# Performance work log

Hardware: AMD Instinct MI355X
Metric: run time of the kernel (lower is better)

The kernel has to match this reference:

```python
import jax, jax.numpy as jnp
import numpy as np


def setup_inputs() -> dict:
    key = jax.random.key(0)
    k1, k2, k3 = jax.random.split(key, 3)
    B, C, H, W = 16, 64, 256, 256
    x = jax.random.normal(k1, (B, C, H, W), dtype=jnp.float32)
    g = jax.random.normal(k2, (B, C, H, W), dtype=jnp.float32)
    gamma = jax.random.normal(k3, (1,), dtype=jnp.float32)
    return {"x": x, "g": g, "gamma": gamma}


def reference(x, g, gamma):
    # x, g: (B, C, H, W); gamma: (1,)
    B, C, H, W = x.shape
    N = H * W
    xq = x.reshape(B, C, N)   # proj_query / proj_value
    gq = g.reshape(B, C, N)

    # channel-channel energy from x: (B, C, C)
    energy = jnp.einsum('bcn,bdn->bcd', xq, xq)
    attention = jax.nn.softmax(energy, axis=-1)

    # channel-channel energy from guide g: (B, C, C)
    energy_guide = jnp.einsum('bcn,bdn->bcd', gq, gq)
    attention_guide = jax.nn.softmax(energy_guide, axis=-1)

    # chained attention: (B, C, C)
    guide_energy = jnp.einsum('bcd,bde->bce', attention, attention_guide)
    guide_energy_new = jnp.max(guide_energy, axis=-1, keepdims=True) - guide_energy
    guide_attention = jax.nn.softmax(guide_energy_new, axis=-1)

    # apply to values and residual
    out = jnp.einsum('bcd,bdn->bcn', guide_attention, xq).reshape(B, C, H, W)
    return gamma[0] * out + x
```

## Files before the change

### kernel.cpp

```cpp
#include <hip/hip_runtime.h>


typedef _Float16 h8 __attribute__((ext_vector_type(8)));
typedef float    f4 __attribute__((ext_vector_type(4)));
typedef __fp16   p2 __attribute__((ext_vector_type(2)));
typedef unsigned long long ull;

#define NB 16
#define NC 64
#define NPIX 65536
#define GRAM_CHUNK 1024
#define PASS_PX 128
#define NPASS (GRAM_CHUNK / PASS_PX)
#define NCHUNK (NPIX / GRAM_CHUNK)
#define ROW_H 136
#define LDS_H (64 * ROW_H + 64)

#define AP_NPX 256
#define XT_ROW 72

__device__ __forceinline__ int rowbase_h(int c) {
    return c * ROW_H + (c >> 3) * 8;
}

__device__ __forceinline__ unsigned int pk(float a, float b) {
    p2 v = __builtin_amdgcn_cvt_pkrtz(a, b);
    return __builtin_bit_cast(unsigned int, v);
}

__global__ __launch_bounds__(256, 6) void gram_kernel(
    const float* __restrict__ x, const float* __restrict__ g,
    float* __restrict__ part)
{
    __shared__ __align__(16) _Float16 buf[LDS_H];

    const int tid = threadIdx.x;
    const int mtx = blockIdx.z;
    const float* src = (mtx ? g : x)
        + (size_t)blockIdx.y * NC * NPIX + (size_t)blockIdx.x * GRAM_CHUNK;

    const int w     = tid >> 6;
    const int lane  = tid & 63;
    const int l15   = lane & 15;
    const int khalf = lane >> 4;
    const int abase_h = rowbase_h(w * 16 + l15);

    const int sq = tid & 31;
    const int sr = tid >> 5;

    f4 acc[4];
    #pragma unroll
    for (int cb = 0; cb < 4; ++cb) acc[cb] = (f4){0.f, 0.f, 0.f, 0.f};

    for (int pass = 0; pass < NPASS; ++pass) {
        const float* ps = src + pass * PASS_PX;
        #pragma unroll
        for (int it = 0; it < 8; ++it) {
            int r = it * 8 + sr;
            f4 v = *(const f4*)(ps + (size_t)r * NPIX + sq * 4);
            ull h = (ull)pk(v.x, v.y) | ((ull)pk(v.z, v.w) << 32);
            *reinterpret_cast<ull*>(&buf[rowbase_h(r) + 4 * sq]) = h;
        }
        __syncthreads();

        #pragma unroll
        for (int ks = 0; ks < 4; ++ks) {
            int koff = ks * 32 + khalf * 8;
            h8 a = *reinterpret_cast<const h8*>(&buf[abase_h + koff]);
            #pragma unroll
            for (int cb = 0; cb < 4; ++cb) {
                h8 bf = *reinterpret_cast<const h8*>(&buf[rowbase_h(cb * 16 + l15) + koff]);
                acc[cb] = __builtin_amdgcn_mfma_f32_16x16x32_f16(a, bf, acc[cb], 0, 0, 0);
            }
        }
        __syncthreads();
    }

    float* po = part + (((size_t)blockIdx.x * NB + blockIdx.y) * 2 + mtx) * 4096;
    #pragma unroll
    for (int cb = 0; cb < 4; ++cb)
        #pragma unroll
        for (int r = 0; r < 4; ++r)
            po[(w * 16 + khalf * 4 + r) * 64 + cb * 16 + l15] = acc[cb][r];
}

__global__ __launch_bounds__(256) void reduce_kernel(
    const float* __restrict__ part, float* __restrict__ ex, float* __restrict__ eg)
{
    const int idx = blockIdx.x * 256 + threadIdx.x;
    const int bm = idx >> 12;
    const int cd = idx & 4095;
    float s = 0.f;
    #pragma unroll 8
    for (int ch = 0; ch < NCHUNK; ++ch)
        s += part[(size_t)ch * (NB * 2 * 4096) + (size_t)bm * 4096 + cd];
    float* dst = (bm & 1) ? eg : ex;
    dst[(bm >> 1) * 4096 + cd] = s;
}

__global__ __launch_bounds__(256) void chain_kernel(
    const float* __restrict__ ex, const float* __restrict__ eg,
    const float* __restrict__ gammap, float* __restrict__ M)
{
    __shared__ float A1[64][68];
    __shared__ float A2[64][68];
    __shared__ float red[64][4];

    const int b = blockIdx.x;
    const int tid = threadIdx.x;

    if (tid < 64) {
        const int c = tid;
        float r[64];
        #pragma unroll
        for (int d = 0; d < 64; ++d) r[d] = ex[b * 4096 + c * 64 + d];
        float mx = r[0];
        #pragma unroll
        for (int d = 1; d < 64; ++d) mx = fmaxf(mx, r[d]);
        float s = 0.f;
        #pragma unroll
        for (int d = 0; d < 64; ++d) { r[d] = expf(r[d] - mx); s += r[d]; }
        float inv = 1.f / s;
        #pragma unroll
        for (int d = 0; d < 64; ++d) A1[c][d] = r[d] * inv;

        #pragma unroll
        for (int d = 0; d < 64; ++d) r[d] = eg[b * 4096 + c * 64 + d];
        mx = r[0];
        #pragma unroll
        for (int d = 1; d < 64; ++d) mx = fmaxf(mx, r[d]);
        s = 0.f;
        #pragma unroll
        for (int d = 0; d < 64; ++d) { r[d] = expf(r[d] - mx); s += r[d]; }
        inv = 1.f / s;
        #pragma unroll
        for (int d = 0; d < 64; ++d) A2[c][d] = r[d] * inv;
    }
    __syncthreads();

    const int c = tid >> 2, sq = tid & 3;
    float ge[16];
    #pragma unroll
    for (int k = 0; k < 16; ++k) ge[k] = 0.f;
    for (int d = 0; d < 64; ++d) {
        float a = A1[c][d];
        const float* row = &A2[d][sq * 16];
        #pragma unroll
        for (int k = 0; k < 16; ++k) ge[k] = fmaf(a, row[k], ge[k]);
    }

    float mx = ge[0];
    #pragma unroll
    for (int k = 1; k < 16; ++k) mx = fmaxf(mx, ge[k]);
    red[c][sq] = mx;
    __syncthreads();
    float gm = fmaxf(fmaxf(red[c][0], red[c][1]), fmaxf(red[c][2], red[c][3]));
    __syncthreads();

    float gen[16];
    #pragma unroll
    for (int k = 0; k < 16; ++k) gen[k] = gm - ge[k];
    float mx2 = gen[0];
    #pragma unroll
    for (int k = 1; k < 16; ++k) mx2 = fmaxf(mx2, gen[k]);
    red[c][sq] = mx2;
    __syncthreads();
    float m2 = fmaxf(fmaxf(red[c][0], red[c][1]), fmaxf(red[c][2], red[c][3]));
    __syncthreads();

    float p[16];
    float s = 0.f;
    #pragma unroll
    for (int k = 0; k < 16; ++k) { p[k] = expf(gen[k] - m2); s += p[k]; }
    red[c][sq] = s;
    __syncthreads();
    float S = red[c][0] + red[c][1] + red[c][2] + red[c][3];

    float gam = gammap[0];
    float invS = 1.f / S;
    #pragma unroll
    for (int k = 0; k < 16; ++k) {
        int e = sq * 16 + k;
        M[b * 4096 + c * 64 + e] = gam * p[k] * invS;
    }
}

__global__ __launch_bounds__(256) void apply_kernel(
    const float* __restrict__ x, const float* __restrict__ M,
    float* __restrict__ out)
{
    __shared__ __align__(16) _Float16 xT[AP_NPX * XT_ROW];
    __shared__ __align__(16) _Float16 Ml[64 * XT_ROW];

    const int tid = threadIdx.x;
    const int b = blockIdx.y;
    const int n0 = blockIdx.x * AP_NPX;
    const float* xb = x + (size_t)b * NC * NPIX + n0;

    #pragma unroll
    for (int it = 0; it < 8; ++it) {
        int e = it * 256 + tid;
        int q  = e & 63;
        int dp = e >> 6;
        f4 va = *(const f4*)(xb + (size_t)(2 * dp)     * NPIX + q * 4);
        f4 vb = *(const f4*)(xb + (size_t)(2 * dp + 1) * NPIX + q * 4);
        #pragma unroll
        for (int j = 0; j < 4; ++j) {
            float aj = (j == 0) ? va.x : (j == 1) ? va.y : (j == 2) ? va.z : va.w;
            float bj = (j == 0) ? vb.x : (j == 1) ? vb.y : (j == 2) ? vb.z : vb.w;
            *reinterpret_cast<unsigned int*>(&xT[(q * 4 + j) * XT_ROW + 2 * dp]) = pk(aj, bj);
        }
    }
    const float* Mb = M + b * 4096;
    #pragma unroll
    for (int it = 0; it < 4; ++it) {
        int e = it * 256 + tid;
        int c  = e >> 4;
        int qq = e & 15;
        f4 mv = *(const f4*)(Mb + c * 64 + qq * 4);
        *reinterpret_cast<unsigned int*>(&Ml[c * XT_ROW + qq * 4])     = pk(mv.x, mv.y);
        *reinterpret_cast<unsigned int*>(&Ml[c * XT_ROW + qq * 4 + 2]) = pk(mv.z, mv.w);
    }
    __syncthreads();

    const int w    = tid >> 6;
    const int lane = tid & 63;
    const int l15  = lane & 15;
    const int kh   = lane >> 4;

    h8 bfrag[4][2];
    #pragma unroll
    for (int nb = 0; nb < 4; ++nb)
        #pragma unroll
        for (int ks = 0; ks < 2; ++ks)
            bfrag[nb][ks] = *reinterpret_cast<const h8*>(
                &xT[(w * 64 + nb * 16 + l15) * XT_ROW + ks * 32 + kh * 8]);

    f4 acc[4][4];
    #pragma unroll
    for (int cb = 0; cb < 4; ++cb)
        #pragma unroll
        for (int nb = 0; nb < 4; ++nb) acc[cb][nb] = (f4){0.f, 0.f, 0.f, 0.f};

    #pragma unroll
    for (int cb = 0; cb < 4; ++cb) {
        #pragma unroll
        for (int ks = 0; ks < 2; ++ks) {
            h8 a = *reinterpret_cast<const h8*>(
                &Ml[(cb * 16 + l15) * XT_ROW + ks * 32 + kh * 8]);
            #pragma unroll
            for (int nb = 0; nb < 4; ++nb)
                acc[cb][nb] = __builtin_amdgcn_mfma_f32_16x16x32_f16(a, bfrag[nb][ks], acc[cb][nb], 0, 0, 0);
        }
    }

    const size_t base = (size_t)b * NC * NPIX + n0 + w * 64;
    #pragma unroll
    for (int cb = 0; cb < 4; ++cb) {
        #pragma unroll
        for (int r = 0; r < 4; ++r) {
            const int row = cb * 16 + kh * 4 + r;
            #pragma unroll
            for (int nb = 0; nb < 4; ++nb) {
                size_t idx = base + (size_t)row * NPIX + nb * 16 + l15;
                out[idx] = acc[cb][nb][r] + x[idx];
            }
        }
    }
}

extern "C" void kernel_launch(void* const* d_in, const int* in_sizes, int n_in,
                              void* d_out, int out_size, void* d_ws, size_t ws_size,
                              hipStream_t stream) {
    const float* x     = (const float*)d_in[0];
    const float* g     = (const float*)d_in[1];
    const float* gamma = (const float*)d_in[2];
    float* out = (float*)d_out;
    float* ws  = (float*)d_ws;

    float* ex = ws;
    float* eg = ws + NB * 4096;
    float* M  = ws + 2 * NB * 4096;

    float* part = out;

    gram_kernel<<<dim3(NCHUNK, NB, 2), 256, 0, stream>>>(x, g, part);
    reduce_kernel<<<512, 256, 0, stream>>>(part, ex, eg);
    chain_kernel<<<NB, 256, 0, stream>>>(ex, eg, gamma, M);
    apply_kernel<<<dim3(NPIX / AP_NPX, NB), 256, 0, stream>>>(x, M, out);
}
```

Baseline: 282.8 us.

## Load whole gram chunk up front with 512-thread blocks and 4x2 wave tiling

The gram kernel now uses 512-thread blocks with a 512-pixel chunk. Each thread issues all sixteen global loads back to back before converting them to fp16 and writing them to LDS, replacing the old loop of eight 128-pixel passes with a sync on each side. The eight waves split the 64x64 output as a 4x2 grid, each running a 16-step MFMA loop over two accumulators. This aims to raise memory-level parallelism and drop per-pass barriers. In exchange it doubles the chunk count, so the partials buffer and the reduce kernel's reads double, and each block needs much more LDS, which lowers the number of resident blocks.

```diff
diff --git a/kernel.cpp b/kernel.cpp
--- a/kernel.cpp
+++ b/kernel.cpp
@@ -9,11 +9,9 @@
 #define NB 16
 #define NC 64
 #define NPIX 65536
-#define GRAM_CHUNK 1024
-#define PASS_PX 128
-#define NPASS (GRAM_CHUNK / PASS_PX)
+#define GRAM_CHUNK 512
 #define NCHUNK (NPIX / GRAM_CHUNK)
-#define ROW_H 136
+#define ROW_H 520
 #define LDS_H (64 * ROW_H + 64)
 
 #define AP_NPX 256
@@ -28,7 +26,7 @@
     return __builtin_bit_cast(unsigned int, v);
 }
 
-__global__ __launch_bounds__(256, 6) void gram_kernel(
+__global__ __launch_bounds__(512, 4) void gram_kernel(
     const float* __restrict__ x, const float* __restrict__ g,
     float* __restrict__ part)
 {
@@ -39,49 +37,67 @@
     const float* src = (mtx ? g : x)
         + (size_t)blockIdx.y * NC * NPIX + (size_t)blockIdx.x * GRAM_CHUNK;
 
+    const int sq = tid & 127;
+    const int sr = tid >> 7;
+
+    f4 t0, t1, t2, t3, t4, t5, t6, t7, t8, t9, t10, t11, t12, t13, t14, t15;
+    {
+        const float* p = src + (size_t)sr * NPIX + sq * 4;
+        const size_t rs = 4 * (size_t)NPIX;
+        t0  = *(const f4*)(p + 0 * rs);   t1  = *(const f4*)(p + 1 * rs);
+        t2  = *(const f4*)(p + 2 * rs);   t3  = *(const f4*)(p + 3 * rs);
+        t4  = *(const f4*)(p + 4 * rs);   t5  = *(const f4*)(p + 5 * rs);
+        t6  = *(const f4*)(p + 6 * rs);   t7  = *(const f4*)(p + 7 * rs);
+        t8  = *(const f4*)(p + 8 * rs);   t9  = *(const f4*)(p + 9 * rs);
+        t10 = *(const f4*)(p + 10 * rs);  t11 = *(const f4*)(p + 11 * rs);
+        t12 = *(const f4*)(p + 12 * rs);  t13 = *(const f4*)(p + 13 * rs);
+        t14 = *(const f4*)(p + 14 * rs);  t15 = *(const f4*)(p + 15 * rs);
+    }
+    asm volatile("" : "+v"(t0), "+v"(t1), "+v"(t2), "+v"(t3));
+    asm volatile("" : "+v"(t4), "+v"(t5), "+v"(t6), "+v"(t7));
+    asm volatile("" : "+v"(t8), "+v"(t9), "+v"(t10), "+v"(t11));
+    asm volatile("" : "+v"(t12), "+v"(t13), "+v"(t14), "+v"(t15));
+
+    #define CVW(T, IT) { \
+        ull h = (ull)pk(T.x, T.y) | ((ull)pk(T.z, T.w) << 32); \
+        *reinterpret_cast<ull*>(&buf[rowbase_h((IT) * 4 + sr) + 4 * sq]) = h; }
+    CVW(t0, 0)  CVW(t1, 1)  CVW(t2, 2)  CVW(t3, 3)
+    CVW(t4, 4)  CVW(t5, 5)  CVW(t6, 6)  CVW(t7, 7)
+    CVW(t8, 8)  CVW(t9, 9)  CVW(t10, 10) CVW(t11, 11)
+    CVW(t12, 12) CVW(t13, 13) CVW(t14, 14) CVW(t15, 15)
+    #undef CVW
+
+    __syncthreads();
+
     const int w     = tid >> 6;
     const int lane  = tid & 63;
     const int l15   = lane & 15;
     const int khalf = lane >> 4;
-    const int abase_h = rowbase_h(w * 16 + l15);
-
-    const int sq = tid & 31;
-    const int sr = tid >> 5;
-
-    f4 acc[4];
-    #pragma unroll
-    for (int cb = 0; cb < 4; ++cb) acc[cb] = (f4){0.f, 0.f, 0.f, 0.f};
-
-    for (int pass = 0; pass < NPASS; ++pass) {
-        const float* ps = src + pass * PASS_PX;
-        #pragma unroll
-        for (int it = 0; it < 8; ++it) {
-            int r = it * 8 + sr;
-            f4 v = *(const f4*)(ps + (size_t)r * NPIX + sq * 4);
-            ull h = (ull)pk(v.x, v.y) | ((ull)pk(v.z, v.w) << 32);
-            *reinterpret_cast<ull*>(&buf[rowbase_h(r) + 4 * sq]) = h;
-        }
-        __syncthreads();
-
-        #pragma unroll
-        for (int ks = 0; ks < 4; ++ks) {
-            int koff = ks * 32 + khalf * 8;
-            h8 a = *reinterpret_cast<const h8*>(&buf[abase_h + koff]);
-            #pragma unroll
-            for (int cb = 0; cb < 4; ++cb) {
-                h8 bf = *reinterpret_cast<const h8*>(&buf[rowbase_h(cb * 16 + l15) + koff]);
-                acc[cb] = __builtin_amdgcn_mfma_f32_16x16x32_f16(a, bf, acc[cb], 0, 0, 0);
-            }
-        }
-        __syncthreads();
+    const int wr    = w >> 1;
+    const int wc    = w & 1;
+    const int abase_h = rowbase_h(wr * 16 + l15);
+    const int bbase0  = rowbase_h((wc * 2 + 0) * 16 + l15);
+    const int bbase1  = rowbase_h((wc * 2 + 1) * 16 + l15);
+
+    f4 acc0 = (f4){0.f, 0.f, 0.f, 0.f};
+    f4 acc1 = (f4){0.f, 0.f, 0.f, 0.f};
+
+    #pragma unroll
+    for (int ks = 0; ks < 16; ++ks) {
+        int koff = ks * 32 + khalf * 8;
+        h8 a  = *reinterpret_cast<const h8*>(&buf[abase_h + koff]);
+        h8 b0 = *reinterpret_cast<const h8*>(&buf[bbase0 + koff]);
+        h8 b1 = *reinterpret_cast<const h8*>(&buf[bbase1 + koff]);
+        acc0 = __builtin_amdgcn_mfma_f32_16x16x32_f16(a, b0, acc0, 0, 0, 0);
+        acc1 = __builtin_amdgcn_mfma_f32_16x16x32_f16(a, b1, acc1, 0, 0, 0);
     }
 
     float* po = part + (((size_t)blockIdx.x * NB + blockIdx.y) * 2 + mtx) * 4096;
     #pragma unroll
-    for (int cb = 0; cb < 4; ++cb)
-        #pragma unroll
-        for (int r = 0; r < 4; ++r)
-            po[(w * 16 + khalf * 4 + r) * 64 + cb * 16 + l15] = acc[cb][r];
+    for (int r = 0; r < 4; ++r) {
+        po[(wr * 16 + khalf * 4 + r) * 64 + wc * 32 + 0 * 16 + l15] = acc0[r];
+        po[(wr * 16 + khalf * 4 + r) * 64 + wc * 32 + 1 * 16 + l15] = acc1[r];
+    }
 }
 
 __global__ __launch_bounds__(256) void reduce_kernel(
@@ -284,7 +300,7 @@
 
     float* part = out;
 
-    gram_kernel<<<dim3(NCHUNK, NB, 2), 256, 0, stream>>>(x, g, part);
+    gram_kernel<<<dim3(NCHUNK, NB, 2), 512, 0, stream>>>(x, g, part);
     reduce_kernel<<<512, 256, 0, stream>>>(part, ex, eg);
     chain_kernel<<<NB, 256, 0, stream>>>(ex, eg, gamma, M);
     apply_kernel<<<dim3(NPIX / AP_NPX, NB), 256, 0, stream>>>(x, M, out);
```

Result: faster. 266.6 us (-5.7%).

## Load whole 512-pixel gram chunk in one pass and store fp16 partial sums

Applied to the files above, without the earlier changes.

The gram kernel now stages an entire 512-pixel chunk for all 64 channels in LDS with a single barrier, replacing the multi-pass loop over 128-pixel slices. It drops the bank-skew padding and the occupancy hint. Partial Gram results are written as fp16, which halves partial-buffer traffic even though the chunk count doubles. The cost is a much larger LDS footprint, roughly 66 KB per block, which lowers occupancy. Partial sums of large magnitude may also lose precision or overflow in fp16.

```diff
diff --git a/kernel.cpp b/kernel.cpp
--- a/kernel.cpp
+++ b/kernel.cpp
@@ -9,28 +9,22 @@
 #define NB 16
 #define NC 64
 #define NPIX 65536
-#define GRAM_CHUNK 1024
-#define PASS_PX 128
-#define NPASS (GRAM_CHUNK / PASS_PX)
+#define GRAM_CHUNK 512
 #define NCHUNK (NPIX / GRAM_CHUNK)
-#define ROW_H 136
-#define LDS_H (64 * ROW_H + 64)
+#define ROW_H 520
+#define LDS_H (64 * ROW_H)
 
 #define AP_NPX 256
 #define XT_ROW 72
-
-__device__ __forceinline__ int rowbase_h(int c) {
-    return c * ROW_H + (c >> 3) * 8;
-}
 
 __device__ __forceinline__ unsigned int pk(float a, float b) {
     p2 v = __builtin_amdgcn_cvt_pkrtz(a, b);
     return __builtin_bit_cast(unsigned int, v);
 }
 
-__global__ __launch_bounds__(256, 6) void gram_kernel(
+__global__ __launch_bounds__(256) void gram_kernel(
     const float* __restrict__ x, const float* __restrict__ g,
-    float* __restrict__ part)
+    _Float16* __restrict__ part)
 {
     __shared__ __align__(16) _Float16 buf[LDS_H];
 
@@ -39,53 +33,51 @@
     const float* src = (mtx ? g : x)
         + (size_t)blockIdx.y * NC * NPIX + (size_t)blockIdx.x * GRAM_CHUNK;
 
-    const int w     = tid >> 6;
-    const int lane  = tid & 63;
+    const int w    = tid >> 6;
+    const int lane = tid & 63;
+
+    #pragma unroll
+    for (int rr = 0; rr < 16; ++rr) {
+        const int r = w * 16 + rr;
+        const float* rp = src + (size_t)r * NPIX + lane * 4;
+        f4 va = *(const f4*)(rp);
+        f4 vb = *(const f4*)(rp + 256);
+        ull ha = (ull)pk(va.x, va.y) | ((ull)pk(va.z, va.w) << 32);
+        ull hb = (ull)pk(vb.x, vb.y) | ((ull)pk(vb.z, vb.w) << 32);
+        *reinterpret_cast<ull*>(&buf[r * ROW_H + lane * 4])       = ha;
+        *reinterpret_cast<ull*>(&buf[r * ROW_H + 256 + lane * 4]) = hb;
+    }
+    __syncthreads();
+
     const int l15   = lane & 15;
     const int khalf = lane >> 4;
-    const int abase_h = rowbase_h(w * 16 + l15);
-
-    const int sq = tid & 31;
-    const int sr = tid >> 5;
+    const int abase = (w * 16 + l15) * ROW_H;
 
     f4 acc[4];
     #pragma unroll
     for (int cb = 0; cb < 4; ++cb) acc[cb] = (f4){0.f, 0.f, 0.f, 0.f};
 
-    for (int pass = 0; pass < NPASS; ++pass) {
-        const float* ps = src + pass * PASS_PX;
-        #pragma unroll
-        for (int it = 0; it < 8; ++it) {
-            int r = it * 8 + sr;
-            f4 v = *(const f4*)(ps + (size_t)r * NPIX + sq * 4);
-            ull h = (ull)pk(v.x, v.y) | ((ull)pk(v.z, v.w) << 32);
-            *reinterpret_cast<ull*>(&buf[rowbase_h(r) + 4 * sq]) = h;
-        }
-        __syncthreads();
-
-        #pragma unroll
-        for (int ks = 0; ks < 4; ++ks) {
-            int koff = ks * 32 + khalf * 8;
-            h8 a = *reinterpret_cast<const h8*>(&buf[abase_h + koff]);
-            #pragma unroll
-            for (int cb = 0; cb < 4; ++cb) {
-                h8 bf = *reinterpret_cast<const h8*>(&buf[rowbase_h(cb * 16 + l15) + koff]);
-                acc[cb] = __builtin_amdgcn_mfma_f32_16x16x32_f16(a, bf, acc[cb], 0, 0, 0);
-            }
-        }
-        __syncthreads();
-    }
-
-    float* po = part + (((size_t)blockIdx.x * NB + blockIdx.y) * 2 + mtx) * 4096;
+    #pragma unroll
+    for (int ks = 0; ks < 16; ++ks) {
+        int koff = ks * 32 + khalf * 8;
+        h8 a = *reinterpret_cast<const h8*>(&buf[abase + koff]);
+        #pragma unroll
+        for (int cb = 0; cb < 4; ++cb) {
+            h8 bf = *reinterpret_cast<const h8*>(&buf[(cb * 16 + l15) * ROW_H + koff]);
+            acc[cb] = __builtin_amdgcn_mfma_f32_16x16x32_f16(a, bf, acc[cb], 0, 0, 0);
+        }
+    }
+
+    _Float16* po = part + (((size_t)blockIdx.x * NB + blockIdx.y) * 2 + mtx) * 4096;
     #pragma unroll
     for (int cb = 0; cb < 4; ++cb)
         #pragma unroll
         for (int r = 0; r < 4; ++r)
-            po[(w * 16 + khalf * 4 + r) * 64 + cb * 16 + l15] = acc[cb][r];
+            po[(w * 16 + khalf * 4 + r) * 64 + cb * 16 + l15] = (_Float16)acc[cb][r];
 }
 
 __global__ __launch_bounds__(256) void reduce_kernel(
-    const float* __restrict__ part, float* __restrict__ ex, float* __restrict__ eg)
+    const _Float16* __restrict__ part, float* __restrict__ ex, float* __restrict__ eg)
 {
     const int idx = blockIdx.x * 256 + threadIdx.x;
     const int bm = idx >> 12;
@@ -93,7 +85,7 @@
     float s = 0.f;
     #pragma unroll 8
     for (int ch = 0; ch < NCHUNK; ++ch)
-        s += part[(size_t)ch * (NB * 2 * 4096) + (size_t)bm * 4096 + cd];
+        s += (float)part[(size_t)ch * (NB * 2 * 4096) + (size_t)bm * 4096 + cd];
     float* dst = (bm & 1) ? eg : ex;
     dst[(bm >> 1) * 4096 + cd] = s;
 }
@@ -282,7 +274,7 @@
     float* eg = ws + NB * 4096;
     float* M  = ws + 2 * NB * 4096;
 
-    float* part = out;
+    _Float16* part = (_Float16*)out;
 
     gram_kernel<<<dim3(NCHUNK, NB, 2), 256, 0, stream>>>(x, g, part);
     reduce_kernel<<<512, 256, 0, stream>>>(part, ex, eg);
```

After: 267.3 us. 1.06x faster.
